# Optimization experiments

Measured on AMD Instinct MI355X. Metric: run time of the kernel, lower is better.

Reference implementation:

```python
import jax, jax.numpy as jnp
import numpy as np

NUM_HEADS = 16
HEAD_DIM = 64


def setup_inputs() -> dict:
    key = jax.random.key(0)
    ks = jax.random.split(key, 9)
    B, S, E = 16, 577, 1024
    return {
        "hidden_states": jax.random.normal(ks[0], (B, S, E), dtype=jnp.float32),
        "q_w": jax.random.normal(ks[1], (E, E), dtype=jnp.float32) * 0.02,
        "q_b": jax.random.normal(ks[2], (E,), dtype=jnp.float32) * 0.02,
        "v_w": jax.random.normal(ks[3], (E, E), dtype=jnp.float32) * 0.02,
        "v_b": jax.random.normal(ks[4], (E,), dtype=jnp.float32) * 0.02,
        "out_w": jax.random.normal(ks[5], (E, E), dtype=jnp.float32) * 0.02,
        "out_b": jax.random.normal(ks[6], (E,), dtype=jnp.float32) * 0.02,
        "share_key": jax.random.normal(ks[7], (1, NUM_HEADS, HEAD_DIM, 1), dtype=jnp.float32) * 0.1,
        "share_bias": jax.random.normal(ks[8], (NUM_HEADS, S, S), dtype=jnp.float32) * 0.05,
        "layer": 10,
    }


def reference(hidden_states, q_w, q_b, v_w, v_b, out_w, out_b, share_key, share_bias, layer):
    # layer >= START_SHARE_LAYER (9): ShareKey.cal_attention branch.
    B, S, E = hidden_states.shape
    H, D = NUM_HEADS, HEAD_DIM
    scale = D ** -0.5

    # projections (torch Linear: x @ W.T + b)
    q = (hidden_states @ q_w.T + q_b) * scale          # [B,S,E]
    v = hidden_states @ v_w.T + v_b                    # [B,S,E]
    q = q.reshape(B, S, H, D).transpose(0, 2, 1, 3)    # [B,H,S,D]
    v = v.reshape(B, S, H, D).transpose(0, 2, 1, 3)    # [B,H,S,D]

    # rank-1 learned-key scores: matmul(q, key[1,H,D,1]) -> [B,H,S,1]
    scores = jnp.einsum("bhsd,hd->bhs", q, share_key[0, :, :, 0])  # [B,H,S]
    # expand along last axis to [B,H,S,S] and add per-layer learned bias
    attn = scores[..., None] + share_bias[None]         # [B,H,S,S]
    attn = jax.nn.softmax(attn, axis=-1)

    # attn @ V, merge heads, output projection
    out = jnp.einsum("bhij,bhjd->bhid", attn, v)        # [B,H,S,D]
    out = out.transpose(0, 2, 1, 3).reshape(B, S, E)
    out = out @ out_w.T + out_b
    return out
```

## Files before the change

### kernel.cpp

```cpp
#include <hip/hip_runtime.h>


typedef __attribute__((ext_vector_type(4))) float f32x4;
typedef __attribute__((ext_vector_type(4))) unsigned int u32x4;

__device__ __forceinline__ unsigned short f2h(float f) {
  union { _Float16 h; unsigned short u; } x;
  x.h = (_Float16)f;
  return x.u;
}

__device__ __forceinline__ void mfma16(f32x4& d, u32x4 a, u32x4 b) {
  asm("v_mfma_f32_16x16x32_f16 %0, %1, %2, %0" : "+v"(d) : "v"(a), "v"(b));
}

__device__ __forceinline__ void gl_lds16(const unsigned short* g, unsigned short* l) {
  __builtin_amdgcn_global_load_lds(
      (const __attribute__((address_space(1))) unsigned int*)g,
      (__attribute__((address_space(3))) unsigned int*)l, 16, 0, 0);
}

__global__ __launch_bounds__(256) void prep_hs_kernel(const float* __restrict__ X,
                                                      unsigned short* __restrict__ Y) {
  int idx = blockIdx.x * 256 + threadIdx.x;
  int n = idx << 2;
  int row = n >> 10;
  int col = n & 1023;
  int b = row / 584;
  int s = row - b * 584;
  unsigned short o0 = 0, o1 = 0, o2 = 0, o3 = 0;
  if (s < 577) {
    const float4 v = *(const float4*)(X + (((size_t)(b * 577 + s)) << 10) + col);
    o0 = f2h(v.x); o1 = f2h(v.y); o2 = f2h(v.z); o3 = f2h(v.w);
  }
  ushort4 o; o.x = o0; o.y = o1; o.z = o2; o.w = o3;
  *(ushort4*)(Y + n) = o;
}

__global__ __launch_bounds__(256) void prep_w_kernel(const float* __restrict__ X,
                                                     unsigned short* __restrict__ Y) {
  int idx = blockIdx.x * 256 + threadIdx.x;
  int n = idx << 2;
  const float4 v = *(const float4*)(X + n);
  ushort4 o; o.x = f2h(v.x); o.y = f2h(v.y); o.z = f2h(v.z); o.w = f2h(v.w);
  *(ushort4*)(Y + n) = o;
}

__global__ __launch_bounds__(256) void softmax_kernel(const float* __restrict__ SB,
                                                      unsigned short* __restrict__ P) {
  const int i = blockIdx.x;
  const int h = blockIdx.y;
  unsigned short* prow = P + ((size_t)h * 640 + i) * 608;
  const int tid = threadIdx.x;
  if (i >= 577) {
    for (int j = tid; j < 608; j += 256) prow[j] = 0;
    return;
  }
  const float* row = SB + ((size_t)h * 577 + i) * 577;
  __shared__ float buf[577];
  __shared__ float redm[4];
  __shared__ float reds[4];
  float lmax = -3.0e38f;
  for (int j = tid; j < 577; j += 256) { float v = row[j]; buf[j] = v; lmax = fmaxf(lmax, v); }
  #pragma unroll
  for (int off = 32; off > 0; off >>= 1) lmax = fmaxf(lmax, __shfl_xor(lmax, off));
  if ((tid & 63) == 0) redm[tid >> 6] = lmax;
  __syncthreads();
  const float m = fmaxf(fmaxf(redm[0], redm[1]), fmaxf(redm[2], redm[3]));
  float lsum = 0.f;
  for (int j = tid; j < 577; j += 256) { float e = __expf(buf[j] - m); buf[j] = e; lsum += e; }
  #pragma unroll
  for (int off = 32; off > 0; off >>= 1) lsum += __shfl_xor(lsum, off);
  if ((tid & 63) == 0) reds[tid >> 6] = lsum;
  __syncthreads();
  const float inv = 1.f / (reds[0] + reds[1] + reds[2] + reds[3]);
  for (int j = tid; j < 608; j += 256)
    prow[j] = (j < 577) ? f2h(buf[j] * inv) : (unsigned short)0;
}

template<int MODE>
__global__ __launch_bounds__(256) void gemm_glds_kernel(
    const unsigned short* __restrict__ A, int lda,
    const unsigned short* __restrict__ B, int ldb,
    const float* __restrict__ bias,
    void* __restrict__ Cv, int ldc, int K)
{
  __shared__ unsigned short As[128 * 32];
  __shared__ unsigned short Bs[128 * 32];
  const int tid  = threadIdx.x;
  const int lane = tid & 63;
  const int w    = tid >> 6;
  const int wm = w >> 1, wn = w & 1;
  const int m0 = blockIdx.x * 128, n0 = blockIdx.y * 128;
  const int hh = (MODE == 1) ? blockIdx.z : 0;
  const int l15 = lane & 15;
  const int lhi = lane >> 4;

  const int lr = lane >> 2;
  const int lc = (lane & 3) << 3;

  if (MODE == 1) A += (size_t)hh * 640 * 608;

  const unsigned short* gA0 = A + (size_t)(m0 + w * 32 + lr) * lda + lc;
  const unsigned short* gA1 = gA0 + (size_t)16 * lda;

  const unsigned short* gB0;
  const unsigned short* gB1;
  if (MODE == 1) {
    const int nb0 = n0 + w * 32 + lr;
    const int nb1 = nb0 + 16;
    gB0 = B + (size_t)(hh * 64 + (nb0 & 63)) * 9344 + (nb0 >> 6) * 584 + lc;
    gB1 = B + (size_t)(hh * 64 + (nb1 & 63)) * 9344 + (nb1 >> 6) * 584 + lc;
  } else {
    gB0 = B + (size_t)(n0 + w * 32 + lr) * ldb + lc;
    gB1 = gB0 + (size_t)16 * ldb;
  }

  unsigned short* lA0 = As + (w * 32) * 32;
  unsigned short* lA1 = As + (w * 32 + 16) * 32;
  unsigned short* lB0 = Bs + (w * 32) * 32;
  unsigned short* lB1 = Bs + (w * 32 + 16) * 32;

  f32x4 acc[4][4] = {};

  for (int k0 = 0; k0 < K; k0 += 32) {
    gl_lds16(gA0 + k0, lA0);
    gl_lds16(gA1 + k0, lA1);
    gl_lds16(gB0 + k0, lB0);
    gl_lds16(gB1 + k0, lB1);
    __syncthreads();
    u32x4 af[4], bv[4];
    #pragma unroll
    for (int i = 0; i < 4; i++)
      af[i] = *(const u32x4*)&As[(wm * 64 + i * 16 + l15) * 32 + (lhi << 3)];
    #pragma unroll
    for (int i = 0; i < 4; i++)
      bv[i] = *(const u32x4*)&Bs[(wn * 64 + i * 16 + l15) * 32 + (lhi << 3)];
    #pragma unroll
    for (int i = 0; i < 4; i++)
      #pragma unroll
      for (int j = 0; j < 4; j++)
        mfma16(acc[i][j], af[i], bv[j]);
    __syncthreads();
  }

  const int rb = m0 + wm * 64 + (lhi << 2);
  const int cb = n0 + wn * 64 + l15;
  #pragma unroll
  for (int i = 0; i < 4; i++) {
    #pragma unroll
    for (int r = 0; r < 4; r++) {
      const int row = rb + i * 16 + r;
      if (MODE == 0) {
        const float rbias = bias[row];
        #pragma unroll
        for (int j = 0; j < 4; j++) {
          const int col = cb + j * 16;
          ((unsigned short*)Cv)[(size_t)row * ldc + col] = f2h(acc[i][j][r] + rbias);
        }
      } else if (MODE == 1) {
        if (row < 577) {
          #pragma unroll
          for (int j = 0; j < 4; j++) {
            const int n = cb + j * 16;
            const int b = n >> 6, d = n & 63;
            ((unsigned short*)Cv)[(((size_t)b * 577 + row) << 10) + hh * 64 + d] =
                f2h(acc[i][j][r]);
          }
        }
      } else {
        if (row < 9232) {
          #pragma unroll
          for (int j = 0; j < 4; j++) {
            const int col = cb + j * 16;
            ((float*)Cv)[(size_t)row * ldc + col] = acc[i][j][r] + bias[col];
          }
        }
      }
    }
  }
}

extern "C" void kernel_launch(void* const* d_in, const int* in_sizes, int n_in,
                              void* d_out, int out_size, void* d_ws, size_t ws_size,
                              hipStream_t stream) {
  (void)in_sizes; (void)n_in; (void)out_size; (void)ws_size;
  const float* hs    = (const float*)d_in[0];
  const float* v_w   = (const float*)d_in[3];
  const float* v_b   = (const float*)d_in[4];
  const float* out_w = (const float*)d_in[5];
  const float* out_b = (const float*)d_in[6];
  const float* sb    = (const float*)d_in[8];
  float* out = (float*)d_out;

  char* ws = (char*)d_ws;
  constexpr size_t HS_SZ = (size_t)9344 * 1024 * 2;
  constexpr size_t W_SZ  = (size_t)1024 * 1024 * 2;
  constexpr size_t VT_SZ = (size_t)1024 * 9344 * 2 + 256;
  unsigned short* hs_f16 = (unsigned short*)(ws);
  unsigned short* vw_f16 = (unsigned short*)(ws + HS_SZ);
  unsigned short* ow_f16 = (unsigned short*)(ws + HS_SZ + W_SZ);
  unsigned short* vt     = (unsigned short*)(ws + HS_SZ + 2 * W_SZ);
  unsigned short* pmat   = (unsigned short*)(ws + HS_SZ + 2 * W_SZ + VT_SZ);

  prep_hs_kernel<<<9344, 256, 0, stream>>>(hs, hs_f16);
  prep_w_kernel<<<1024, 256, 0, stream>>>(v_w, vw_f16);
  prep_w_kernel<<<1024, 256, 0, stream>>>(out_w, ow_f16);
  softmax_kernel<<<dim3(640, 16), 256, 0, stream>>>(sb, pmat);
  gemm_glds_kernel<0><<<dim3(8, 73), 256, 0, stream>>>(vw_f16, 1024, hs_f16, 1024, v_b,
                                                       (void*)vt, 9344, 1024);
  gemm_glds_kernel<1><<<dim3(5, 8, 16), 256, 0, stream>>>(pmat, 608, vt, 0, nullptr,
                                                          (void*)hs_f16, 0, 608);
  gemm_glds_kernel<2><<<dim3(73, 8), 256, 0, stream>>>(hs_f16, 1024, ow_f16, 1024, out_b,
                                                       (void*)out, 1024, 1024);
}
```

Measured before the change: 250.6 us.

## Double-buffer LDS tiles in GEMMs and remap blocks across XCDs

Splits the shared-memory tiles into two buffers so the next K-slice is loaded via global_load_lds while MFMAs run on the current one. Also flattens the launch grid to 1D and remaps block IDs so consecutive tiles sharing operands land on the same XCD for better L2 reuse. Doubles LDS usage per block, which may reduce occupancy, and the overlap depends on how the compiler places wait counts before barriers.

```diff
diff --git a/kernel.cpp b/kernel.cpp
--- a/kernel.cpp
+++ b/kernel.cpp
@@ -79,31 +79,35 @@
 }
 
 template<int MODE>
-__global__ __launch_bounds__(256) void gemm_glds_kernel(
+__global__ __launch_bounds__(256) void gemm_db_kernel(
     const unsigned short* __restrict__ A, int lda,
     const unsigned short* __restrict__ B, int ldb,
     const float* __restrict__ bias,
     void* __restrict__ Cv, int ldc, int K)
 {
-  __shared__ unsigned short As[128 * 32];
-  __shared__ unsigned short Bs[128 * 32];
+  __shared__ unsigned short As0[128 * 32];
+  __shared__ unsigned short Bs0[128 * 32];
+  __shared__ unsigned short As1[128 * 32];
+  __shared__ unsigned short Bs1[128 * 32];
   const int tid  = threadIdx.x;
   const int lane = tid & 63;
   const int w    = tid >> 6;
   const int wm = w >> 1, wn = w & 1;
-  const int m0 = blockIdx.x * 128, n0 = blockIdx.y * 128;
-  const int hh = (MODE == 1) ? blockIdx.z : 0;
-  const int l15 = lane & 15;
-  const int lhi = lane >> 4;
-
-  const int lr = lane >> 2;
-  const int lc = (lane & 3) << 3;
-
-  if (MODE == 1) A += (size_t)hh * 640 * 608;
-
-  const unsigned short* gA0 = A + (size_t)(m0 + w * 32 + lr) * lda + lc;
+  const int l15 = lane & 15, lhi = lane >> 4;
+  const int lr = lane >> 2, lc = (lane & 3) << 3;
+
+  const int nwg8 = (int)gridDim.x >> 3;
+  const int orig = blockIdx.x;
+  const int id = (orig & 7) * nwg8 + (orig >> 3);
+  int mt, nt, hh = 0;
+  if (MODE == 1)      { hh = id / 40; const int r = id - hh * 40; nt = r & 7; mt = r >> 3; }
+  else if (MODE == 0) { mt = id & 7;  nt = id >> 3; }
+  else                { nt = id & 7;  mt = id >> 3; }
+  const int m0 = mt * 128, n0 = nt * 128;
+
+  const unsigned short* Abase = (MODE == 1) ? A + (size_t)hh * 640 * 608 : A;
+  const unsigned short* gA0 = Abase + (size_t)(m0 + w * 32 + lr) * lda + lc;
   const unsigned short* gA1 = gA0 + (size_t)16 * lda;
-
   const unsigned short* gB0;
   const unsigned short* gB1;
   if (MODE == 1) {
@@ -116,33 +120,47 @@
     gB1 = gB0 + (size_t)16 * ldb;
   }
 
-  unsigned short* lA0 = As + (w * 32) * 32;
-  unsigned short* lA1 = As + (w * 32 + 16) * 32;
-  unsigned short* lB0 = Bs + (w * 32) * 32;
-  unsigned short* lB1 = Bs + (w * 32 + 16) * 32;
-
   f32x4 acc[4][4] = {};
-
-  for (int k0 = 0; k0 < K; k0 += 32) {
-    gl_lds16(gA0 + k0, lA0);
-    gl_lds16(gA1 + k0, lA1);
-    gl_lds16(gB0 + k0, lB0);
-    gl_lds16(gB1 + k0, lB1);
+  const int NT = K >> 5;
+
+#define STAGE(AS, BS, k0)                         \
+  do {                                            \
+    gl_lds16(gA0 + (k0), (AS) + w * 1024);        \
+    gl_lds16(gA1 + (k0), (AS) + w * 1024 + 512);  \
+    gl_lds16(gB0 + (k0), (BS) + w * 1024);        \
+    gl_lds16(gB1 + (k0), (BS) + w * 1024 + 512);  \
+  } while (0)
+
+#define COMPUTE(AS, BS)                                                        \
+  do {                                                                         \
+    u32x4 af[4], bv[4];                                                        \
+    _Pragma("unroll")                                                          \
+    for (int i = 0; i < 4; i++)                                                \
+      af[i] = *(const u32x4*)&(AS)[(wm * 64 + i * 16 + l15) * 32 + (lhi << 3)];\
+    _Pragma("unroll")                                                          \
+    for (int i = 0; i < 4; i++)                                                \
+      bv[i] = *(const u32x4*)&(BS)[(wn * 64 + i * 16 + l15) * 32 + (lhi << 3)];\
+    _Pragma("unroll")                                                          \
+    for (int i = 0; i < 4; i++)                                                \
+      _Pragma("unroll")                                                        \
+      for (int j = 0; j < 4; j++)                                              \
+        mfma16(acc[i][j], af[i], bv[j]);                                       \
+  } while (0)
+
+  STAGE(As0, Bs0, 0);
+  __syncthreads();
+  for (int kt = 0; kt < NT; kt += 2) {
+    if (kt + 1 < NT) STAGE(As1, Bs1, (kt + 1) << 5);
+    COMPUTE(As0, Bs0);
     __syncthreads();
-    u32x4 af[4], bv[4];
-    #pragma unroll
-    for (int i = 0; i < 4; i++)
-      af[i] = *(const u32x4*)&As[(wm * 64 + i * 16 + l15) * 32 + (lhi << 3)];
-    #pragma unroll
-    for (int i = 0; i < 4; i++)
-      bv[i] = *(const u32x4*)&Bs[(wn * 64 + i * 16 + l15) * 32 + (lhi << 3)];
-    #pragma unroll
-    for (int i = 0; i < 4; i++)
-      #pragma unroll
-      for (int j = 0; j < 4; j++)
-        mfma16(acc[i][j], af[i], bv[j]);
-    __syncthreads();
-  }
+    if (kt + 1 < NT) {
+      if (kt + 2 < NT) STAGE(As0, Bs0, (kt + 2) << 5);
+      COMPUTE(As1, Bs1);
+      __syncthreads();
+    }
+  }
+#undef STAGE
+#undef COMPUTE
 
   const int rb = m0 + wm * 64 + (lhi << 2);
   const int cb = n0 + wn * 64 + l15;
@@ -207,10 +225,10 @@
   prep_w_kernel<<<1024, 256, 0, stream>>>(v_w, vw_f16);
   prep_w_kernel<<<1024, 256, 0, stream>>>(out_w, ow_f16);
   softmax_kernel<<<dim3(640, 16), 256, 0, stream>>>(sb, pmat);
-  gemm_glds_kernel<0><<<dim3(8, 73), 256, 0, stream>>>(vw_f16, 1024, hs_f16, 1024, v_b,
-                                                       (void*)vt, 9344, 1024);
-  gemm_glds_kernel<1><<<dim3(5, 8, 16), 256, 0, stream>>>(pmat, 608, vt, 0, nullptr,
-                                                          (void*)hs_f16, 0, 608);
-  gemm_glds_kernel<2><<<dim3(73, 8), 256, 0, stream>>>(hs_f16, 1024, ow_f16, 1024, out_b,
-                                                       (void*)out, 1024, 1024);
-}
+  gemm_db_kernel<0><<<584, 256, 0, stream>>>(vw_f16, 1024, hs_f16, 1024, v_b,
+                                             (void*)vt, 9344, 1024);
+  gemm_db_kernel<1><<<640, 256, 0, stream>>>(pmat, 608, vt, 0, nullptr,
+                                             (void*)hs_f16, 0, 608);
+  gemm_db_kernel<2><<<584, 256, 0, stream>>>(hs_f16, 1024, ow_f16, 1024, out_b,
+                                             (void*)out, 1024, 1024);
+}
```

After: 213.6 us. 14.8% less time.
